# Kernel tuning notes

Measured on AMD Instinct MI355X. Metric: run time of the kernel, lower is better.

Reference implementation:

```python
import jax, jax.numpy as jnp
import numpy as np

EMBED_DIM = 1024
NUM_HEADS = 16
HEAD_DIM = EMBED_DIM // NUM_HEADS
T, B = 2048, 2


def setup_inputs() -> dict:
    key = jax.random.key(0)
    ks = jax.random.split(key, 12)
    s = 1.0 / np.sqrt(EMBED_DIM)
    x = jax.random.normal(ks[0], (T, B, EMBED_DIM), dtype=jnp.float32)
    time_decay = jax.random.uniform(ks[1], (T, B, 1), dtype=jnp.float32)
    # causal mask: masked_fill where mask == 0
    attn_mask = jnp.tril(jnp.ones((T, T), dtype=jnp.int32))
    Wq = jax.random.uniform(ks[2], (EMBED_DIM, EMBED_DIM), jnp.float32, -s, s)
    bq = jax.random.uniform(ks[3], (EMBED_DIM,), jnp.float32, -s, s)
    Wk = jax.random.uniform(ks[4], (EMBED_DIM, EMBED_DIM), jnp.float32, -s, s)
    bk = jax.random.uniform(ks[5], (EMBED_DIM,), jnp.float32, -s, s)
    Wv = jax.random.uniform(ks[6], (EMBED_DIM, EMBED_DIM), jnp.float32, -s, s)
    bv = jax.random.uniform(ks[7], (EMBED_DIM,), jnp.float32, -s, s)
    Wo = jax.random.uniform(ks[8], (EMBED_DIM, EMBED_DIM), jnp.float32, -s, s)
    bo = jax.random.uniform(ks[9], (EMBED_DIM,), jnp.float32, -s, s)
    return {"x": x, "time_decay": time_decay, "attn_mask": attn_mask,
            "Wq": Wq, "bq": bq, "Wk": Wk, "bk": bk,
            "Wv": Wv, "bv": bv, "Wo": Wo, "bo": bo}


def reference(x, time_decay, attn_mask, Wq, bq, Wk, bk, Wv, bv, Wo, bo):
    t, b, e = x.shape
    h, d = NUM_HEADS, HEAD_DIM
    # linear (torch: y = x @ W.T + b), then split heads -> (B, H, T, D)
    def proj(W, bias):
        y = jnp.einsum('tbe,fe->tbf', x, W) + bias
        return y.reshape(t, b, h, d).transpose(1, 2, 0, 3)
    Q, K, V = proj(Wq, bq), proj(Wk, bk), proj(Wv, bv)
    scores = jnp.einsum('bhqd,bhkd->bhqk', Q, K) / np.sqrt(d).astype(jnp.float32)
    scores = jnp.where(attn_mask == 0, jnp.float32(-1e9), scores)
    attn = jax.nn.softmax(scores, axis=-1)
    out = jnp.einsum('bhqk,bhkd->bhqd', attn, V)      # (B,H,T,D)
    out = out.transpose(2, 0, 1, 3).reshape(t, b, e)   # (T,B,E)
    out = jnp.einsum('tbe,fe->tbf', out, Wo) + bo
    return out * time_decay
```

## Files before the change

### kernel.cpp

```cpp
#include <hip/hip_runtime.h>


typedef unsigned short u16;
typedef __attribute__((ext_vector_type(8))) short bf16x8_t;
typedef __attribute__((ext_vector_type(4))) float fx4_t;

#define T_SEQ 2048
#define BATCH 2
#define EMB   1024
#define NH    16
#define HD    64
#define MROWS (T_SEQ * BATCH)

#define EXP2F(x) __builtin_amdgcn_exp2f(x)

__device__ __forceinline__ float bf2f(u16 u) {
  union { unsigned int i; float f; } v;
  v.i = ((unsigned int)u) << 16;
  return v.f;
}
__device__ __forceinline__ u16 f2bf(float f) {
  union { float f; unsigned int i; } v;
  v.f = f;
  unsigned int x = v.i;
  unsigned int r = (x + 0x7fffu + ((x >> 16) & 1u)) >> 16;
  return (u16)r;
}

__device__ __forceinline__ void glds16(const void* g, void* l) {
  __builtin_amdgcn_global_load_lds(
      (const __attribute__((address_space(1))) unsigned int*)g,
      (__attribute__((address_space(3))) unsigned int*)l, 16, 0, 0);
}

__global__ void cvt_all(const float* __restrict__ x,
                        const float* __restrict__ wq, const float* __restrict__ wk,
                        const float* __restrict__ wv, const float* __restrict__ wo,
                        u16* __restrict__ xb,
                        u16* __restrict__ wqb, u16* __restrict__ wkb,
                        u16* __restrict__ wvb, u16* __restrict__ wob) {
  int i = blockIdx.x * blockDim.x + threadIdx.x;
  const float* src; u16* dst; int off;
  if (i < 1048576)      { src = x;  dst = xb;  off = i; }
  else if (i < 1310720) { src = wq; dst = wqb; off = i - 1048576; }
  else if (i < 1572864) { src = wk; dst = wkb; off = i - 1310720; }
  else if (i < 1835008) { src = wv; dst = wvb; off = i - 1572864; }
  else                  { src = wo; dst = wob; off = i - 1835008; }
  float4 v = ((const float4*)src)[off];
  ushort4 o;
  o.x = f2bf(v.x); o.y = f2bf(v.y); o.z = f2bf(v.z); o.w = f2bf(v.w);
  ((ushort4*)dst)[off] = o;
}

__global__ __launch_bounds__(256, 2) void gemm_qkv(
    const u16* __restrict__ xb,
    const u16* __restrict__ wq, const u16* __restrict__ wk, const u16* __restrict__ wv,
    const float* __restrict__ bq, const float* __restrict__ bk, const float* __restrict__ bv,
    u16* __restrict__ Qh, u16* __restrict__ Kh, u16* __restrict__ VTg) {
  __shared__ short As[128 * 64];
  __shared__ short Bs[128 * 64];

  const int z = blockIdx.z;
  const u16* W = (z == 0) ? wq : (z == 1) ? wk : wv;
  const float* bias = (z == 0) ? bq : (z == 1) ? bk : bv;

  const int tid = threadIdx.x;
  const int bm = blockIdx.x, bn = blockIdx.y;
  const int lane = tid & 63, w = tid >> 6;
  const int wm = w >> 1, wn = w & 1;
  const int lr = lane & 15, quad = lane >> 4;
  const int r0 = lane >> 3, c8 = (lane & 7) * 8;

  fx4_t acc[4][4];
#pragma unroll
  for (int i = 0; i < 4; i++)
#pragma unroll
    for (int j = 0; j < 4; j++) acc[i][j] = (fx4_t){0.f, 0.f, 0.f, 0.f};

  for (int k0 = 0; k0 < EMB; k0 += 64) {
#pragma unroll
    for (int i = 0; i < 4; i++) {
      const int rr = w * 32 + i * 8;
      glds16(xb + (size_t)(bm * 128 + rr + r0) * EMB + k0 + c8, &As[rr * 64]);
      glds16(W  + (size_t)(bn * 128 + rr + r0) * EMB + k0 + c8, &Bs[rr * 64]);
    }
    __syncthreads();
#pragma unroll
    for (int ks = 0; ks < 2; ++ks) {
      bf16x8_t a[4], b[4];
      const int goff = (ks * 4 + quad) * 8;
#pragma unroll
      for (int i = 0; i < 4; i++) a[i] = *(const bf16x8_t*)&As[(wm * 64 + i * 16 + lr) * 64 + goff];
#pragma unroll
      for (int j = 0; j < 4; j++) b[j] = *(const bf16x8_t*)&Bs[(wn * 64 + j * 16 + lr) * 64 + goff];
#pragma unroll
      for (int i = 0; i < 4; i++)
#pragma unroll
        for (int j = 0; j < 4; j++)
          acc[i][j] = __builtin_amdgcn_mfma_f32_16x16x32_bf16(a[i], b[j], acc[i][j], 0, 0, 0);
    }
    __syncthreads();
  }

#pragma unroll
  for (int i = 0; i < 4; i++) {
#pragma unroll
    for (int j = 0; j < 4; j++) {
      const int n = bn * 128 + wn * 64 + j * 16 + lr;
      const float bsv = bias[n];
      const int h = n >> 6, d = n & 63;
#pragma unroll
      for (int r = 0; r < 4; r++) {
        const int m = bm * 128 + wm * 64 + i * 16 + quad * 4 + r;
        const int t = m >> 1, bb = m & 1;
        float v = acc[i][j][r] + bsv;
        if (z == 2) {
          VTg[((size_t)(bb * NH + h) * HD + d) * T_SEQ + t] = f2bf(v);
        } else {
          u16* dst = (z == 0) ? Qh : Kh;
          dst[((size_t)(bb * NH + h) * T_SEQ + t) * HD + d] = f2bf(v);
        }
      }
    }
  }
}

__global__ __launch_bounds__(256, 2) void gemm_out(
    const u16* __restrict__ Ob, const u16* __restrict__ wo,
    const float* __restrict__ bo, const float* __restrict__ td,
    float* __restrict__ out) {
  __shared__ short As[64 * 64];
  __shared__ short Bs[128 * 64];

  const int tid = threadIdx.x;
  const int bm = blockIdx.x, bn = blockIdx.y;
  const int lane = tid & 63, w = tid >> 6;
  const int wm = w >> 1, wn = w & 1;
  const int lr = lane & 15, quad = lane >> 4;
  const int r0 = lane >> 3, c8 = (lane & 7) * 8;

  fx4_t acc[2][4];
#pragma unroll
  for (int i = 0; i < 2; i++)
#pragma unroll
    for (int j = 0; j < 4; j++) acc[i][j] = (fx4_t){0.f, 0.f, 0.f, 0.f};

  for (int k0 = 0; k0 < EMB; k0 += 64) {
#pragma unroll
    for (int i = 0; i < 2; i++) {
      const int rr = w * 16 + i * 8;
      glds16(Ob + (size_t)(bm * 64 + rr + r0) * EMB + k0 + c8, &As[rr * 64]);
    }
#pragma unroll
    for (int i = 0; i < 4; i++) {
      const int rr = w * 32 + i * 8;
      glds16(wo + (size_t)(bn * 128 + rr + r0) * EMB + k0 + c8, &Bs[rr * 64]);
    }
    __syncthreads();
#pragma unroll
    for (int ks = 0; ks < 2; ++ks) {
      bf16x8_t a[2], b[4];
      const int goff = (ks * 4 + quad) * 8;
#pragma unroll
      for (int i = 0; i < 2; i++) a[i] = *(const bf16x8_t*)&As[(wm * 32 + i * 16 + lr) * 64 + goff];
#pragma unroll
      for (int j = 0; j < 4; j++) b[j] = *(const bf16x8_t*)&Bs[(wn * 64 + j * 16 + lr) * 64 + goff];
#pragma unroll
      for (int i = 0; i < 2; i++)
#pragma unroll
        for (int j = 0; j < 4; j++)
          acc[i][j] = __builtin_amdgcn_mfma_f32_16x16x32_bf16(a[i], b[j], acc[i][j], 0, 0, 0);
    }
    __syncthreads();
  }

#pragma unroll
  for (int i = 0; i < 2; i++) {
#pragma unroll
    for (int j = 0; j < 4; j++) {
      const int n = bn * 128 + wn * 64 + j * 16 + lr;
      const float bsv = bo[n];
#pragma unroll
      for (int r = 0; r < 4; r++) {
        const int m = bm * 64 + wm * 32 + i * 16 + quad * 4 + r;
        out[(size_t)m * EMB + n] = (acc[i][j][r] + bsv) * td[m];
      }
    }
  }
}

__global__ __launch_bounds__(256, 3) void attn_mfma3(
    const u16* __restrict__ Qh, const u16* __restrict__ Kh, const u16* __restrict__ VTg,
    u16* __restrict__ Ob) {
  __shared__ short Kd[2][64 * 64];
  __shared__ short Vd[2][64 * 64];
  __shared__ short Ps[4][16 * 72];

  const int blk = blockIdx.x;
  const int bh = blk & 31;
  const int j = blk >> 5;
  const int qt = (j & 1) ? (31 - (j >> 1)) : (j >> 1);
  const int qb = qt * 64;

  const int tid = threadIdx.x;
  const int w = tid >> 6, lane = tid & 63;
  const int lr = lane & 15, quad = lane >> 4;
  const int r0 = lane >> 3, c8 = (lane & 7) * 8;

  const u16* Qb = Qh + (size_t)bh * T_SEQ * HD;
  const u16* Kb = Kh + (size_t)bh * T_SEQ * HD;
  const u16* VTb = VTg + (size_t)bh * HD * T_SEQ;

  const float QSCALE = 0.18033688f;
  bf16x8_t qf[2];
#pragma unroll
  for (int ks = 0; ks < 2; ks++) {
    bf16x8_t v = *(const bf16x8_t*)(Qb + (size_t)(qb + w * 16 + lr) * HD + ks * 32 + quad * 8);
    bf16x8_t o;
#pragma unroll
    for (int e = 0; e < 8; e++) o[e] = (short)f2bf(bf2f((u16)v[e]) * QSCALE);
    qf[ks] = o;
  }

  fx4_t acc_o[4];
#pragma unroll
  for (int dn = 0; dn < 4; dn++) acc_o[dn] = (fx4_t){0.f, 0.f, 0.f, 0.f};
  float m_i = -1e30f, l_i = 0.f;

#define STAGE(kt_, buf_)                                                          \
  {                                                                               \
    const int k0_ = (kt_) * 64;                                                   \
    _Pragma("unroll")                                                             \
    for (int i = 0; i < 2; i++) {                                                 \
      const int rr = w * 16 + i * 8;                                              \
      glds16(Kb + (size_t)(k0_ + rr + r0) * HD + c8, &Kd[buf_][rr * 64]);         \
      glds16(VTb + (size_t)(rr + r0) * T_SEQ + k0_ + c8, &Vd[buf_][rr * 64]);     \
    }                                                                             \
  }

  const int nkt = qt + 1;
  STAGE(0, 0);
  __syncthreads();

  for (int kt = 0; kt < nkt; kt++) {
    const int buf = kt & 1;
    if (kt + 1 < nkt) STAGE(kt + 1, buf ^ 1);

    fx4_t st[4];
#pragma unroll
    for (int nt = 0; nt < 4; nt++) st[nt] = (fx4_t){0.f, 0.f, 0.f, 0.f};
#pragma unroll
    for (int ks = 0; ks < 2; ks++) {
#pragma unroll
      for (int nt = 0; nt < 4; nt++) {
        bf16x8_t kf = *(const bf16x8_t*)&Kd[buf][(nt * 16 + lr) * 64 + ks * 32 + quad * 8];
        st[nt] = __builtin_amdgcn_mfma_f32_16x16x32_bf16(kf, qf[ks], st[nt], 0, 0, 0);
      }
    }

    if (kt == qt) {
#pragma unroll
      for (int nt = 0; nt < 4; nt++)
#pragma unroll
        for (int r = 0; r < 4; r++)
          if (nt * 16 + quad * 4 + r > w * 16 + lr) st[nt][r] = -1e30f;
    }

    float rmax = -1e30f;
#pragma unroll
    for (int nt = 0; nt < 4; nt++)
#pragma unroll
      for (int r = 0; r < 4; r++) rmax = fmaxf(rmax, st[nt][r]);
    rmax = fmaxf(rmax, __shfl_xor(rmax, 16));
    rmax = fmaxf(rmax, __shfl_xor(rmax, 32));
    const float mn = fmaxf(m_i, rmax);
    const float alpha = EXP2F(m_i - mn);
    m_i = mn;
    float rsum = 0.f;
#pragma unroll
    for (int nt = 0; nt < 4; nt++) {
#pragma unroll
      for (int r = 0; r < 4; r++) {
        float e = EXP2F(st[nt][r] - mn);
        st[nt][r] = e;
        rsum += e;
      }
    }
    rsum += __shfl_xor(rsum, 16);
    rsum += __shfl_xor(rsum, 32);
    l_i = l_i * alpha + rsum;

    short* Pw = Ps[w];
#pragma unroll
    for (int nt = 0; nt < 4; nt++) {
      short4 pv;
      pv.x = (short)f2bf(st[nt][0]);
      pv.y = (short)f2bf(st[nt][1]);
      pv.z = (short)f2bf(st[nt][2]);
      pv.w = (short)f2bf(st[nt][3]);
      *(short4*)&Pw[lr * 72 + nt * 16 + quad * 4] = pv;
    }

#pragma unroll
    for (int r = 0; r < 4; r++) {
      const float a_r = __shfl(alpha, quad * 4 + r);
#pragma unroll
      for (int dn = 0; dn < 4; dn++) acc_o[dn][r] *= a_r;
    }

#pragma unroll
    for (int ks = 0; ks < 2; ks++) {
      bf16x8_t pf = *(const bf16x8_t*)&Pw[lr * 72 + ks * 32 + quad * 8];
#pragma unroll
      for (int dn = 0; dn < 4; dn++) {
        bf16x8_t vf = *(const bf16x8_t*)&Vd[buf][(dn * 16 + lr) * 64 + ks * 32 + quad * 8];
        acc_o[dn] = __builtin_amdgcn_mfma_f32_16x16x32_bf16(pf, vf, acc_o[dn], 0, 0, 0);
      }
    }

    __syncthreads();
  }
#undef STAGE

  const float inv = 1.0f / l_i;
  const int b = bh >> 4, h = bh & 15;
#pragma unroll
  for (int r = 0; r < 4; r++) {
    const float inv_r = __shfl(inv, quad * 4 + r);
    const int t = qb + w * 16 + quad * 4 + r;
#pragma unroll
    for (int dn = 0; dn < 4; dn++) {
      const int d = dn * 16 + lr;
      Ob[(size_t)(t * BATCH + b) * EMB + h * HD + d] = f2bf(acc_o[dn][r] * inv_r);
    }
  }
}

extern "C" void kernel_launch(void* const* d_in, const int* in_sizes, int n_in,
                              void* d_out, int out_size, void* d_ws, size_t ws_size,
                              hipStream_t stream) {
  const float* x  = (const float*)d_in[0];
  const float* td = (const float*)d_in[1];
  const float* Wq = (const float*)d_in[3];
  const float* bq = (const float*)d_in[4];
  const float* Wk = (const float*)d_in[5];
  const float* bk = (const float*)d_in[6];
  const float* Wv = (const float*)d_in[7];
  const float* bv = (const float*)d_in[8];
  const float* Wo = (const float*)d_in[9];
  const float* bo = (const float*)d_in[10];
  float* out = (float*)d_out;

  char* ws = (char*)d_ws;
  u16* xb  = (u16*)(ws + 0);
  u16* wqb = (u16*)(ws + ((size_t)8  << 20));
  u16* wkb = (u16*)(ws + ((size_t)10 << 20));
  u16* wvb = (u16*)(ws + ((size_t)12 << 20));
  u16* wob = (u16*)(ws + ((size_t)14 << 20));
  u16* Qh  = (u16*)(ws + ((size_t)16 << 20));
  u16* Kh  = (u16*)(ws + ((size_t)24 << 20));
  u16* VTg = (u16*)(ws + ((size_t)32 << 20));
  u16* Ob  = xb;

  cvt_all<<<8192, 256, 0, stream>>>(x, Wq, Wk, Wv, Wo, xb, wqb, wkb, wvb, wob);

  gemm_qkv<<<dim3(MROWS / 128, EMB / 128, 3), 256, 0, stream>>>(
      xb, wqb, wkb, wvb, bq, bk, bv, Qh, Kh, VTg);

  attn_mfma3<<<1024, 256, 0, stream>>>(Qh, Kh, VTg, Ob);

  gemm_out<<<dim3(MROWS / 64, EMB / 128), 256, 0, stream>>>(Ob, wob, bo, td, out);
}
```

Before: 229.8 us.

## Swizzle LDS tiles, coalesce V-transpose stores, and double attention query tile

```diff
diff --git a/kernel.cpp b/kernel.cpp
--- a/kernel.cpp
+++ b/kernel.cpp
@@ -32,6 +32,7 @@
       (const __attribute__((address_space(1))) unsigned int*)g,
       (__attribute__((address_space(3))) unsigned int*)l, 16, 0, 0);
 }
+
 
 __global__ void cvt_all(const float* __restrict__ x,
                         const float* __restrict__ wq, const float* __restrict__ wk,
@@ -69,7 +70,9 @@
   const int lane = tid & 63, w = tid >> 6;
   const int wm = w >> 1, wn = w & 1;
   const int lr = lane & 15, quad = lane >> 4;
-  const int r0 = lane >> 3, c8 = (lane & 7) * 8;
+  const int r0 = lane >> 3;
+  const int c8s = ((lane & 7) ^ r0) * 8;
+  const int sw = (lr & 7);
 
   fx4_t acc[4][4];
 #pragma unroll
@@ -81,44 +84,67 @@
 #pragma unroll
     for (int i = 0; i < 4; i++) {
       const int rr = w * 32 + i * 8;
-      glds16(xb + (size_t)(bm * 128 + rr + r0) * EMB + k0 + c8, &As[rr * 64]);
-      glds16(W  + (size_t)(bn * 128 + rr + r0) * EMB + k0 + c8, &Bs[rr * 64]);
+      const int ml = bm * 128 + rr + r0;
+      const int grow = (z == 2) ? (((ml & 2047) << 1) | (ml >> 11)) : ml;
+      glds16(xb + (size_t)grow * EMB + k0 + c8s, &As[rr * 64]);
+      glds16(W + (size_t)(bn * 128 + rr + r0) * EMB + k0 + c8s, &Bs[rr * 64]);
     }
     __syncthreads();
 #pragma unroll
     for (int ks = 0; ks < 2; ++ks) {
       bf16x8_t a[4], b[4];
-      const int goff = (ks * 4 + quad) * 8;
-#pragma unroll
-      for (int i = 0; i < 4; i++) a[i] = *(const bf16x8_t*)&As[(wm * 64 + i * 16 + lr) * 64 + goff];
-#pragma unroll
-      for (int j = 0; j < 4; j++) b[j] = *(const bf16x8_t*)&Bs[(wn * 64 + j * 16 + lr) * 64 + goff];
 #pragma unroll
       for (int i = 0; i < 4; i++)
-#pragma unroll
-        for (int j = 0; j < 4; j++)
-          acc[i][j] = __builtin_amdgcn_mfma_f32_16x16x32_bf16(a[i], b[j], acc[i][j], 0, 0, 0);
+        a[i] = *(const bf16x8_t*)&As[(wm * 64 + i * 16 + lr) * 64 + (((ks * 4 + quad) ^ sw) * 8)];
+#pragma unroll
+      for (int j = 0; j < 4; j++)
+        b[j] = *(const bf16x8_t*)&Bs[(wn * 64 + j * 16 + lr) * 64 + (((ks * 4 + quad) ^ sw) * 8)];
+      if (z == 2) {
+#pragma unroll
+        for (int i = 0; i < 4; i++)
+#pragma unroll
+          for (int j = 0; j < 4; j++)
+            acc[i][j] = __builtin_amdgcn_mfma_f32_16x16x32_bf16(b[j], a[i], acc[i][j], 0, 0, 0);
+      } else {
+#pragma unroll
+        for (int i = 0; i < 4; i++)
+#pragma unroll
+          for (int j = 0; j < 4; j++)
+            acc[i][j] = __builtin_amdgcn_mfma_f32_16x16x32_bf16(a[i], b[j], acc[i][j], 0, 0, 0);
+      }
     }
     __syncthreads();
   }
 
-#pragma unroll
-  for (int i = 0; i < 4; i++) {
-#pragma unroll
-    for (int j = 0; j < 4; j++) {
-      const int n = bn * 128 + wn * 64 + j * 16 + lr;
-      const float bsv = bias[n];
-      const int h = n >> 6, d = n & 63;
-#pragma unroll
-      for (int r = 0; r < 4; r++) {
-        const int m = bm * 128 + wm * 64 + i * 16 + quad * 4 + r;
-        const int t = m >> 1, bb = m & 1;
-        float v = acc[i][j][r] + bsv;
-        if (z == 2) {
-          VTg[((size_t)(bb * NH + h) * HD + d) * T_SEQ + t] = f2bf(v);
-        } else {
-          u16* dst = (z == 0) ? Qh : Kh;
-          dst[((size_t)(bb * NH + h) * T_SEQ + t) * HD + d] = f2bf(v);
+  if (z == 2) {
+#pragma unroll
+    for (int i = 0; i < 4; i++) {
+#pragma unroll
+      for (int j = 0; j < 4; j++) {
+#pragma unroll
+        for (int r = 0; r < 4; r++) {
+          const int n = bn * 128 + wn * 64 + j * 16 + quad * 4 + r;
+          const int ml = bm * 128 + wm * 64 + i * 16 + lr;
+          const int t = ml & 2047, bb = ml >> 11;
+          const int h = n >> 6, d = n & 63;
+          VTg[((size_t)(bb * NH + h) * HD + d) * T_SEQ + t] = f2bf(acc[i][j][r] + bias[n]);
+        }
+      }
+    }
+  } else {
+    u16* dst = (z == 0) ? Qh : Kh;
+#pragma unroll
+    for (int i = 0; i < 4; i++) {
+#pragma unroll
+      for (int j = 0; j < 4; j++) {
+        const int n = bn * 128 + wn * 64 + j * 16 + lr;
+        const float bsv = bias[n];
+        const int h = n >> 6, d = n & 63;
+#pragma unroll
+        for (int r = 0; r < 4; r++) {
+          const int m = bm * 128 + wm * 64 + i * 16 + quad * 4 + r;
+          const int t = m >> 1, bb = m & 1;
+          dst[((size_t)(bb * NH + h) * T_SEQ + t) * HD + d] = f2bf(acc[i][j][r] + bsv);
         }
       }
     }
@@ -137,7 +163,9 @@
   const int lane = tid & 63, w = tid >> 6;
   const int wm = w >> 1, wn = w & 1;
   const int lr = lane & 15, quad = lane >> 4;
-  const int r0 = lane >> 3, c8 = (lane & 7) * 8;
+  const int r0 = lane >> 3;
+  const int c8s = ((lane & 7) ^ r0) * 8;
+  const int sw = (lr & 7);
 
   fx4_t acc[2][4];
 #pragma unroll
@@ -149,22 +177,23 @@
 #pragma unroll
     for (int i = 0; i < 2; i++) {
       const int rr = w * 16 + i * 8;
-      glds16(Ob + (size_t)(bm * 64 + rr + r0) * EMB + k0 + c8, &As[rr * 64]);
+      glds16(Ob + (size_t)(bm * 64 + rr + r0) * EMB + k0 + c8s, &As[rr * 64]);
     }
 #pragma unroll
     for (int i = 0; i < 4; i++) {
       const int rr = w * 32 + i * 8;
-      glds16(wo + (size_t)(bn * 128 + rr + r0) * EMB + k0 + c8, &Bs[rr * 64]);
+      glds16(wo + (size_t)(bn * 128 + rr + r0) * EMB + k0 + c8s, &Bs[rr * 64]);
     }
     __syncthreads();
 #pragma unroll
     for (int ks = 0; ks < 2; ++ks) {
       bf16x8_t a[2], b[4];
-      const int goff = (ks * 4 + quad) * 8;
-#pragma unroll
-      for (int i = 0; i < 2; i++) a[i] = *(const bf16x8_t*)&As[(wm * 32 + i * 16 + lr) * 64 + goff];
-#pragma unroll
-      for (int j = 0; j < 4; j++) b[j] = *(const bf16x8_t*)&Bs[(wn * 64 + j * 16 + lr) * 64 + goff];
+#pragma unroll
+      for (int i = 0; i < 2; i++)
+        a[i] = *(const bf16x8_t*)&As[(wm * 32 + i * 16 + lr) * 64 + (((ks * 4 + quad) ^ sw) * 8)];
+#pragma unroll
+      for (int j = 0; j < 4; j++)
+        b[j] = *(const bf16x8_t*)&Bs[(wn * 64 + j * 16 + lr) * 64 + (((ks * 4 + quad) ^ sw) * 8)];
 #pragma unroll
       for (int i = 0; i < 2; i++)
 #pragma unroll
@@ -189,43 +218,49 @@
   }
 }
 
-__global__ __launch_bounds__(256, 3) void attn_mfma3(
+__global__ __launch_bounds__(256, 2) void attn_mfma4(
     const u16* __restrict__ Qh, const u16* __restrict__ Kh, const u16* __restrict__ VTg,
     u16* __restrict__ Ob) {
   __shared__ short Kd[2][64 * 64];
   __shared__ short Vd[2][64 * 64];
-  __shared__ short Ps[4][16 * 72];
+  __shared__ short Ps[4][32 * 72];
 
   const int blk = blockIdx.x;
   const int bh = blk & 31;
   const int j = blk >> 5;
-  const int qt = (j & 1) ? (31 - (j >> 1)) : (j >> 1);
-  const int qb = qt * 64;
+  const int qt = (j < 8) ? j : (23 - j);
+  const int qb = qt * 128;
 
   const int tid = threadIdx.x;
   const int w = tid >> 6, lane = tid & 63;
   const int lr = lane & 15, quad = lane >> 4;
-  const int r0 = lane >> 3, c8 = (lane & 7) * 8;
+  const int r0 = lane >> 3;
+  const int c8s = ((lane & 7) ^ r0) * 8;
+  const int sw = (lr & 7);
 
   const u16* Qb = Qh + (size_t)bh * T_SEQ * HD;
   const u16* Kb = Kh + (size_t)bh * T_SEQ * HD;
   const u16* VTb = VTg + (size_t)bh * HD * T_SEQ;
 
   const float QSCALE = 0.18033688f;
-  bf16x8_t qf[2];
-#pragma unroll
-  for (int ks = 0; ks < 2; ks++) {
-    bf16x8_t v = *(const bf16x8_t*)(Qb + (size_t)(qb + w * 16 + lr) * HD + ks * 32 + quad * 8);
-    bf16x8_t o;
-#pragma unroll
-    for (int e = 0; e < 8; e++) o[e] = (short)f2bf(bf2f((u16)v[e]) * QSCALE);
-    qf[ks] = o;
-  }
-
-  fx4_t acc_o[4];
-#pragma unroll
-  for (int dn = 0; dn < 4; dn++) acc_o[dn] = (fx4_t){0.f, 0.f, 0.f, 0.f};
-  float m_i = -1e30f, l_i = 0.f;
+  bf16x8_t qf[2][2];
+#pragma unroll
+  for (int mt = 0; mt < 2; mt++)
+#pragma unroll
+    for (int ks = 0; ks < 2; ks++) {
+      bf16x8_t v = *(const bf16x8_t*)(Qb + (size_t)(qb + w * 32 + mt * 16 + lr) * HD + ks * 32 + quad * 8);
+      bf16x8_t o;
+#pragma unroll
+      for (int e = 0; e < 8; e++) o[e] = (short)f2bf(bf2f((u16)v[e]) * QSCALE);
+      qf[mt][ks] = o;
+    }
+
+  fx4_t acc_o[2][4];
+#pragma unroll
+  for (int mt = 0; mt < 2; mt++)
+#pragma unroll
+    for (int dn = 0; dn < 4; dn++) acc_o[mt][dn] = (fx4_t){0.f, 0.f, 0.f, 0.f};
+  float m_i[2] = {-1e30f, -1e30f}, l_i[2] = {0.f, 0.f};
 
 #define STAGE(kt_, buf_)                                                          \
   {                                                                               \
@@ -233,105 +268,133 @@
     _Pragma("unroll")                                                             \
     for (int i = 0; i < 2; i++) {                                                 \
       const int rr = w * 16 + i * 8;                                              \
-      glds16(Kb + (size_t)(k0_ + rr + r0) * HD + c8, &Kd[buf_][rr * 64]);         \
-      glds16(VTb + (size_t)(rr + r0) * T_SEQ + k0_ + c8, &Vd[buf_][rr * 64]);     \
+      glds16(Kb + (size_t)(k0_ + rr + r0) * HD + c8s, &Kd[buf_][rr * 64]);        \
+      glds16(VTb + (size_t)(rr + r0) * T_SEQ + k0_ + c8s, &Vd[buf_][rr * 64]);    \
     }                                                                             \
   }
 
-  const int nkt = qt + 1;
+  const int nkt = 2 * qt + 2;
   STAGE(0, 0);
   __syncthreads();
 
   for (int kt = 0; kt < nkt; kt++) {
     const int buf = kt & 1;
     if (kt + 1 < nkt) STAGE(kt + 1, buf ^ 1);
-
-    fx4_t st[4];
-#pragma unroll
-    for (int nt = 0; nt < 4; nt++) st[nt] = (fx4_t){0.f, 0.f, 0.f, 0.f};
-#pragma unroll
-    for (int ks = 0; ks < 2; ks++) {
-#pragma unroll
-      for (int nt = 0; nt < 4; nt++) {
-        bf16x8_t kf = *(const bf16x8_t*)&Kd[buf][(nt * 16 + lr) * 64 + ks * 32 + quad * 8];
-        st[nt] = __builtin_amdgcn_mfma_f32_16x16x32_bf16(kf, qf[ks], st[nt], 0, 0, 0);
-      }
-    }
-
-    if (kt == qt) {
-#pragma unroll
-      for (int nt = 0; nt < 4; nt++)
-#pragma unroll
-        for (int r = 0; r < 4; r++)
-          if (nt * 16 + quad * 4 + r > w * 16 + lr) st[nt][r] = -1e30f;
-    }
-
-    float rmax = -1e30f;
-#pragma unroll
-    for (int nt = 0; nt < 4; nt++)
-#pragma unroll
-      for (int r = 0; r < 4; r++) rmax = fmaxf(rmax, st[nt][r]);
-    rmax = fmaxf(rmax, __shfl_xor(rmax, 16));
-    rmax = fmaxf(rmax, __shfl_xor(rmax, 32));
-    const float mn = fmaxf(m_i, rmax);
-    const float alpha = EXP2F(m_i - mn);
-    m_i = mn;
-    float rsum = 0.f;
-#pragma unroll
-    for (int nt = 0; nt < 4; nt++) {
-#pragma unroll
-      for (int r = 0; r < 4; r++) {
-        float e = EXP2F(st[nt][r] - mn);
-        st[nt][r] = e;
-        rsum += e;
-      }
-    }
-    rsum += __shfl_xor(rsum, 16);
-    rsum += __shfl_xor(rsum, 32);
-    l_i = l_i * alpha + rsum;
-
-    short* Pw = Ps[w];
-#pragma unroll
-    for (int nt = 0; nt < 4; nt++) {
-      short4 pv;
-      pv.x = (short)f2bf(st[nt][0]);
-      pv.y = (short)f2bf(st[nt][1]);
-      pv.z = (short)f2bf(st[nt][2]);
-      pv.w = (short)f2bf(st[nt][3]);
-      *(short4*)&Pw[lr * 72 + nt * 16 + quad * 4] = pv;
-    }
-
+    const int k0 = kt * 64;
+
+    if (k0 <= qb + w * 32 + 31) {
+      fx4_t st[2][4];
+#pragma unroll
+      for (int mt = 0; mt < 2; mt++)
+#pragma unroll
+        for (int nt = 0; nt < 4; nt++) st[mt][nt] = (fx4_t){0.f, 0.f, 0.f, 0.f};
+#pragma unroll
+      for (int ks = 0; ks < 2; ks++) {
+#pragma unroll
+        for (int nt = 0; nt < 4; nt++) {
+          bf16x8_t kf = *(const bf16x8_t*)&Kd[buf][(nt * 16 + lr) * 64 + (((ks * 4 + quad) ^ sw) * 8)];
+#pragma unroll
+          for (int mt = 0; mt < 2; mt++)
+            st[mt][nt] = __builtin_amdgcn_mfma_f32_16x16x32_bf16(kf, qf[mt][ks], st[mt][nt], 0, 0, 0);
+        }
+      }
+
+#pragma unroll
+      for (int mt = 0; mt < 2; mt++) {
+        const int qrow = qb + w * 32 + mt * 16 + lr;
+        if (k0 + 63 > qb + w * 32 + mt * 16) {
+#pragma unroll
+          for (int nt = 0; nt < 4; nt++)
+#pragma unroll
+            for (int r = 0; r < 4; r++)
+              if (k0 + nt * 16 + quad * 4 + r > qrow) st[mt][nt][r] = -1e30f;
+        }
+      }
+
+      float alpha[2];
+#pragma unroll
+      for (int mt = 0; mt < 2; mt++) {
+        float rmax = -1e30f;
+#pragma unroll
+        for (int nt = 0; nt < 4; nt++)
+#pragma unroll
+          for (int r = 0; r < 4; r++) rmax = fmaxf(rmax, st[mt][nt][r]);
+        rmax = fmaxf(rmax, __shfl_xor(rmax, 16));
+        rmax = fmaxf(rmax, __shfl_xor(rmax, 32));
+        const float mn = fmaxf(m_i[mt], rmax);
+        alpha[mt] = EXP2F(m_i[mt] - mn);
+        m_i[mt] = mn;
+        float rsum = 0.f;
+#pragma unroll
+        for (int nt = 0; nt < 4; nt++) {
+#pragma unroll
+          for (int r = 0; r < 4; r++) {
+            float e = EXP2F(st[mt][nt][r] - mn);
+            st[mt][nt][r] = e;
+            rsum += e;
+          }
+        }
+        rsum += __shfl_xor(rsum, 16);
+        rsum += __shfl_xor(rsum, 32);
+        l_i[mt] = l_i[mt] * alpha[mt] + rsum;
+      }
+
+      short* Pw = Ps[w];
+#pragma unroll
+      for (int mt = 0; mt < 2; mt++)
+#pragma unroll
+        for (int nt = 0; nt < 4; nt++) {
+          short4 pv;
+          pv.x = (short)f2bf(st[mt][nt][0]);
+          pv.y = (short)f2bf(st[mt][nt][1]);
+          pv.z = (short)f2bf(st[mt][nt][2]);
+          pv.w = (short)f2bf(st[mt][nt][3]);
+          *(short4*)&Pw[(mt * 16 + lr) * 72 + nt * 16 + quad * 4] = pv;
+        }
+
+#pragma unroll
+      for (int mt = 0; mt < 2; mt++)
+#pragma unroll
+        for (int r = 0; r < 4; r++) {
+          const float a_r = __shfl(alpha[mt], quad * 4 + r);
+#pragma unroll
+          for (int dn = 0; dn < 4; dn++) acc_o[mt][dn][r] *= a_r;
+        }
+
+#pragma unroll
+      for (int ks = 0; ks < 2; ks++) {
+        bf16x8_t pf[2], vf[4];
+#pragma unroll
+        for (int mt = 0; mt < 2; mt++)
+          pf[mt] = *(const bf16x8_t*)&Pw[(mt * 16 + lr) * 72 + ks * 32 + quad * 8];
+#pragma unroll
+        for (int dn = 0; dn < 4; dn++)
+          vf[dn] = *(const bf16x8_t*)&Vd[buf][(dn * 16 + lr) * 64 + (((ks * 4 + quad) ^ sw) * 8)];
+#pragma unroll
+        for (int mt = 0; mt < 2; mt++)
+#pragma unroll
+          for (int dn = 0; dn < 4; dn++)
+            acc_o[mt][dn] = __builtin_amdgcn_mfma_f32_16x16x32_bf16(pf[mt], vf[dn], acc_o[mt][dn], 0, 0, 0);
+      }
+    }
+
+    __syncthreads();
+  }
+#undef STAGE
+
+  const int b = bh >> 4, h = bh & 15;
+#pragma unroll
+  for (int mt = 0; mt < 2; mt++) {
+    const float inv = 1.0f / l_i[mt];
 #pragma unroll
     for (int r = 0; r < 4; r++) {
-      const float a_r = __shfl(alpha, quad * 4 + r);
-#pragma unroll
-      for (int dn = 0; dn < 4; dn++) acc_o[dn][r] *= a_r;
-    }
-
-#pragma unroll
-    for (int ks = 0; ks < 2; ks++) {
-      bf16x8_t pf = *(const bf16x8_t*)&Pw[lr * 72 + ks * 32 + quad * 8];
+      const float inv_r = __shfl(inv, quad * 4 + r);
+      const int t = qb + w * 32 + mt * 16 + quad * 4 + r;
 #pragma unroll
       for (int dn = 0; dn < 4; dn++) {
-        bf16x8_t vf = *(const bf16x8_t*)&Vd[buf][(dn * 16 + lr) * 64 + ks * 32 + quad * 8];
-        acc_o[dn] = __builtin_amdgcn_mfma_f32_16x16x32_bf16(pf, vf, acc_o[dn], 0, 0, 0);
-      }
-    }
-
-    __syncthreads();
-  }
-#undef STAGE
-
-  const float inv = 1.0f / l_i;
-  const int b = bh >> 4, h = bh & 15;
-#pragma unroll
-  for (int r = 0; r < 4; r++) {
-    const float inv_r = __shfl(inv, quad * 4 + r);
-    const int t = qb + w * 16 + quad * 4 + r;
-#pragma unroll
-    for (int dn = 0; dn < 4; dn++) {
-      const int d = dn * 16 + lr;
-      Ob[(size_t)(t * BATCH + b) * EMB + h * HD + d] = f2bf(acc_o[dn][r] * inv_r);
+        const int d = dn * 16 + lr;
+        Ob[(size_t)(t * BATCH + b) * EMB + h * HD + d] = f2bf(acc_o[mt][dn][r] * inv_r);
+      }
     }
   }
 }
@@ -367,7 +430,7 @@
   gemm_qkv<<<dim3(MROWS / 128, EMB / 128, 3), 256, 0, stream>>>(
       xb, wqb, wkb, wvb, bq, bk, bv, Qh, Kh, VTg);
 
-  attn_mfma3<<<1024, 256, 0, stream>>>(Qh, Kh, VTg, Ob);
+  attn_mfma4<<<512, 256, 0, stream>>>(Qh, Kh, VTg, Ob);
 
   gemm_out<<<dim3(MROWS / 64, EMB / 128), 256, 0, stream>>>(Ob, wob, bo, td, out);
 }
```

After: 216.4 us. -5.8%, faster.
